# Kernel optimization log

Measured on AMD Instinct MI355X. Metric: run time of the kernel, lower is better.

Reference implementation:

```python
import jax, jax.numpy as jnp
import numpy as np

D = 1024
H = 16
HD = D // H

def setup_inputs() -> dict:
    key = jax.random.key(0)
    ks = jax.random.split(key, 5)
    scale = 1.0 / np.sqrt(D)
    x = jax.random.normal(ks[0], (2, 2048, D), dtype=jnp.float32)
    W_qkv = jax.random.uniform(ks[1], (D, 3 * D), minval=-scale, maxval=scale, dtype=jnp.float32)
    b_qkv = jax.random.uniform(ks[2], (3 * D,), minval=-scale, maxval=scale, dtype=jnp.float32)
    W_out = jax.random.uniform(ks[3], (D, D), minval=-scale, maxval=scale, dtype=jnp.float32)
    b_out = jax.random.uniform(ks[4], (D,), minval=-scale, maxval=scale, dtype=jnp.float32)
    return {"x": x, "W_qkv": W_qkv, "b_qkv": b_qkv, "W_out": W_out, "b_out": b_out}

def reference(x, W_qkv, b_qkv, W_out, b_out):
    B, S, _ = x.shape
    qkv = x @ W_qkv + b_qkv  # [B,S,3D]
    qkv = qkv.reshape(B, S, 3, H, HD).transpose(2, 0, 3, 1, 4)  # [3,B,H,S,HD]
    q, k, v = qkv[0], qkv[1], qkv[2]
    scores = jnp.einsum('bhsd,bhtd->bhst', q, k) / jnp.sqrt(jnp.float32(HD))
    probs = jax.nn.softmax(scores, axis=-1)
    attn = jnp.einsum('bhst,bhtd->bhsd', probs, v)  # [B,H,S,HD]
    attn = attn.transpose(0, 2, 1, 3).reshape(B, S, D)
    return attn @ W_out + b_out
```

## Files before the change

### kernel.cpp

```cpp
#include <hip/hip_runtime.h>


typedef short bf16x8 __attribute__((ext_vector_type(8)));
typedef short bf16x4 __attribute__((ext_vector_type(4)));
typedef float f32x4 __attribute__((ext_vector_type(4)));

#if __has_builtin(__builtin_amdgcn_mfma_f32_16x16x16_bf16)
#define MFMA16(a, b, c) __builtin_amdgcn_mfma_f32_16x16x16_bf16(a, b, c, 0, 0, 0)
#else
#define MFMA16(a, b, c) __builtin_amdgcn_mfma_f32_16x16x16bf16_1k(a, b, c, 0, 0, 0)
#endif

__device__ __forceinline__ unsigned short f2bf(float f) {
  unsigned u = __float_as_uint(f);
  u = (u + 0x7fffu + ((u >> 16) & 1u)) >> 16;
  return (unsigned short)u;
}
__device__ __forceinline__ unsigned pack_bf2(float lo, float hi) {
  unsigned a = __float_as_uint(lo) + 0x8000u;
  unsigned b = __float_as_uint(hi) + 0x8000u;
  return __builtin_amdgcn_perm(b, a, 0x07060302);
}
__device__ __forceinline__ void load_lds16(const unsigned short* g, unsigned short* l) {
  __builtin_amdgcn_global_load_lds(
      (const __attribute__((address_space(1))) void*)g,
      (__attribute__((address_space(3))) void*)l, 16, 0, 0);
}

__global__ __launch_bounds__(256) void cvt_f32_bf16(
    const float* __restrict__ in, unsigned short* __restrict__ out, int n)
{
  const int i = (blockIdx.x * 256 + threadIdx.x) * 8;
  if (i >= n) return;
  float4 f0 = *(const float4*)(in + i);
  float4 f1 = *(const float4*)(in + i + 4);
  union { unsigned short u[8]; uint4 v; } pk;
  pk.u[0] = f2bf(f0.x); pk.u[1] = f2bf(f0.y); pk.u[2] = f2bf(f0.z); pk.u[3] = f2bf(f0.w);
  pk.u[4] = f2bf(f1.x); pk.u[5] = f2bf(f1.y); pk.u[6] = f2bf(f1.z); pk.u[7] = f2bf(f1.w);
  *(uint4*)(out + i) = pk.v;
}

__global__ __launch_bounds__(256) void transpose_cvt(
    const float* __restrict__ in, unsigned short* __restrict__ out, int R, int C)
{
  __shared__ float tile[64][65];
  const int tid = threadIdx.x;
  const int r0 = blockIdx.y * 64, c0 = blockIdx.x * 64;
  {
    const int rr = tid >> 4;
    const int cc = (tid & 15) * 4;
#pragma unroll
    for (int it = 0; it < 4; ++it) {
      float4 f = *(const float4*)&in[(size_t)(r0 + rr + 16 * it) * C + c0 + cc];
      tile[rr + 16 * it][cc + 0] = f.x;
      tile[rr + 16 * it][cc + 1] = f.y;
      tile[rr + 16 * it][cc + 2] = f.z;
      tile[rr + 16 * it][cc + 3] = f.w;
    }
  }
  __syncthreads();
  {
    const int cr = tid >> 2;
    const int rk = (tid & 3) * 16;
    union { unsigned short u[16]; uint4 v[2]; } pk;
#pragma unroll
    for (int j = 0; j < 16; ++j) pk.u[j] = f2bf(tile[rk + j][cr]);
    uint4* dst = (uint4*)&out[(size_t)(c0 + cr) * R + r0 + rk];
    dst[0] = pk.v[0];
    dst[1] = pk.v[1];
  }
}

template <int MODE>
__global__ __launch_bounds__(256) void gemm_mfma(
    const unsigned short* __restrict__ A,
    const unsigned short* __restrict__ Bt,
    const float* __restrict__ bias,
    void* __restrict__ Cout, unsigned short* __restrict__ vT,
    int M, int N, int K)
{
  __shared__ unsigned short As[128][32];
  __shared__ unsigned short Bs[128][32];
  const int tid = threadIdx.x;
  const int wave = tid >> 6, lane = tid & 63;
  const int l16 = lane & 15, quad = lane >> 4;
  const int m0 = blockIdx.y * 128, n0 = blockIdx.x * 128;
  const int wm = (wave & 1) * 64, wn = (wave >> 1) * 64;
  const int lr = lane >> 2;
  const int lc = (lane & 3) * 8;

  f32x4 acc[4][4] = {};

  for (int k0 = 0; k0 < K; k0 += 32) {
    __syncthreads();
    load_lds16(&A [(size_t)(m0 + 16 * wave + lr) * K + k0 + lc],      &As[16 * wave][0]);
    load_lds16(&A [(size_t)(m0 + 64 + 16 * wave + lr) * K + k0 + lc], &As[64 + 16 * wave][0]);
    load_lds16(&Bt[(size_t)(n0 + 16 * wave + lr) * K + k0 + lc],      &Bs[16 * wave][0]);
    load_lds16(&Bt[(size_t)(n0 + 64 + 16 * wave + lr) * K + k0 + lc], &Bs[64 + 16 * wave][0]);
    __syncthreads();

    bf16x8 af[4], bfr[4];
#pragma unroll
    for (int mi = 0; mi < 4; ++mi)
      af[mi] = *(const bf16x8*)&As[wm + 16 * mi + l16][quad * 8];
#pragma unroll
    for (int ni = 0; ni < 4; ++ni)
      bfr[ni] = *(const bf16x8*)&Bs[wn + 16 * ni + l16][quad * 8];
#pragma unroll
    for (int mi = 0; mi < 4; ++mi)
#pragma unroll
      for (int ni = 0; ni < 4; ++ni)
        acc[mi][ni] = __builtin_amdgcn_mfma_f32_16x16x32_bf16(
            af[mi], bfr[ni], acc[mi][ni], 0, 0, 0);
  }

  const float SCQ = 0.18033688f;
#pragma unroll
  for (int ni = 0; ni < 4; ++ni) {
    const int colb = n0 + wn + 16 * ni;
    const int col = colb + l16;
    const float bv = bias[col];
    if (MODE == 0) {
#pragma unroll
      for (int mi = 0; mi < 4; ++mi)
#pragma unroll
        for (int i = 0; i < 4; ++i) {
          const int row = m0 + wm + 16 * mi + quad * 4 + i;
          ((float*)Cout)[(size_t)row * N + col] = acc[mi][ni][i] + bv;
        }
    } else if (colb < 1024) {
#pragma unroll
      for (int mi = 0; mi < 4; ++mi)
#pragma unroll
        for (int i = 0; i < 4; ++i) {
          const int row = m0 + wm + 16 * mi + quad * 4 + i;
          ((unsigned short*)Cout)[(size_t)row * N + col] = f2bf((acc[mi][ni][i] + bv) * SCQ);
        }
    } else if (colb < 2048) {
#pragma unroll
      for (int mi = 0; mi < 4; ++mi)
#pragma unroll
        for (int i = 0; i < 4; ++i) {
          const int row = m0 + wm + 16 * mi + quad * 4 + i;
          ((unsigned short*)Cout)[(size_t)row * N + col] = f2bf(acc[mi][ni][i] + bv);
        }
    } else {
      const int h = (col - 2048) >> 6, d = col & 63;
#pragma unroll
      for (int mi = 0; mi < 4; ++mi) {
        const int row = m0 + wm + 16 * mi + quad * 4;
        const int bb = row >> 11, t = row & 2047;
        unsigned short* dst = &vT[((size_t)(bb * 16 + h) * 64 + d) * 2048 + t];
        *(unsigned*)(dst)     = pack_bf2(acc[mi][ni][0] + bv, acc[mi][ni][1] + bv);
        *(unsigned*)(dst + 2) = pack_bf2(acc[mi][ni][2] + bv, acc[mi][ni][3] + bv);
      }
    }
  }
}

__global__ __launch_bounds__(256, 2) void attn_mfma(
    const unsigned short* __restrict__ qkv,
    const unsigned short* __restrict__ vT,
    unsigned short* __restrict__ attn_out)
{
  __shared__ unsigned short Ks[2][4096];
  __shared__ unsigned short Vs[2][4096];

  const int tid = threadIdx.x;
  const int wave = tid >> 6, lane = tid & 63;
  const int l16 = lane & 15, quad = lane >> 4;
  const int bh = blockIdx.y, b = bh >> 4, h = bh & 15;
  const int s0 = blockIdx.x * 128 + wave * 32;

  const unsigned short* qb = qkv + (size_t)(b * 2048) * 3072 + h * 64;
  const unsigned short* kb = qb + 1024;
  const unsigned short* vb = vT + (size_t)bh * 64 * 2048;

  const int srow = lane >> 3;
  const int schunk = ((lane & 7) ^ srow) * 8;
  const int r0a = wave * 16;
  const unsigned short* kg0 = kb + (size_t)(r0a + srow) * 3072 + schunk;
  const unsigned short* kg1 = kg0 + (size_t)8 * 3072;
  const unsigned short* vg0 = vb + (size_t)(r0a + srow) * 2048 + schunk;
  const unsigned short* vg1 = vg0 + (size_t)8 * 2048;

#define STAGE_KV(buf, t0)                                            \
  do {                                                               \
    load_lds16(kg0 + (size_t)(t0) * 3072, &Ks[buf][r0a * 64]);       \
    load_lds16(kg1 + (size_t)(t0) * 3072, &Ks[buf][(r0a + 8) * 64]); \
    load_lds16(vg0 + (t0),                &Vs[buf][r0a * 64]);       \
    load_lds16(vg1 + (t0),                &Vs[buf][(r0a + 8) * 64]); \
  } while (0)

  STAGE_KV(0, 0);

  bf16x8 qf[2][2];
#pragma unroll
  for (int mt = 0; mt < 2; ++mt)
#pragma unroll
    for (int ks = 0; ks < 2; ++ks)
      qf[mt][ks] = *(const bf16x8*)&qb[(size_t)(s0 + 16 * mt + l16) * 3072 + 32 * ks + quad * 8];

  f32x4 O[2][4] = {};
  f32x4 lacc[2] = {};
  const bf16x4 ones4 = {(short)0x3F80, (short)0x3F80, (short)0x3F80, (short)0x3F80};
  const int sw = l16 & 7;
  const int h2 = quad >> 1, h1 = (quad & 1) * 4;

  for (int it = 0; it < 32; ++it) {
    const int cur = it & 1;
    __syncthreads();
    if (it < 31) STAGE_KV(1 - cur, (it + 1) * 64);

    bf16x8 kf[4][2];
#pragma unroll
    for (int nt = 0; nt < 4; ++nt) {
      const int rb = (16 * nt + l16) * 64;
      kf[nt][0] = *(const bf16x8*)&Ks[cur][rb + ((quad ^ sw) * 8)];
      kf[nt][1] = *(const bf16x8*)&Ks[cur][rb + (((4 + quad) ^ sw) * 8)];
    }

    bf16x4 vf[4][4];
#pragma unroll
    for (int nd = 0; nd < 4; ++nd) {
      const int rb = (16 * nd + l16) * 64;
#pragma unroll
      for (int c = 0; c < 4; ++c)
        vf[nd][c] = *(const bf16x4*)&Vs[cur][rb + (((2 * c + h2) ^ sw) * 8 + h1)];
    }

    f32x4 sf[4][2];
#pragma unroll
    for (int nt = 0; nt < 4; ++nt)
#pragma unroll
      for (int mt = 0; mt < 2; ++mt) {
        f32x4 c = {0.0f, 0.0f, 0.0f, 0.0f};
        c = __builtin_amdgcn_mfma_f32_16x16x32_bf16(kf[nt][0], qf[mt][0], c, 0, 0, 0);
        c = __builtin_amdgcn_mfma_f32_16x16x32_bf16(kf[nt][1], qf[mt][1], c, 0, 0, 0);
        sf[nt][mt] = c;
      }

    bf16x4 pp[2][4];
#pragma unroll
    for (int mt = 0; mt < 2; ++mt)
#pragma unroll
      for (int nt = 0; nt < 4; ++nt) {
        const float p0 = __builtin_amdgcn_exp2f(sf[nt][mt][0]);
        const float p1 = __builtin_amdgcn_exp2f(sf[nt][mt][1]);
        const float p2 = __builtin_amdgcn_exp2f(sf[nt][mt][2]);
        const float p3 = __builtin_amdgcn_exp2f(sf[nt][mt][3]);
        uint2 w;
        w.x = pack_bf2(p0, p1);
        w.y = pack_bf2(p2, p3);
        pp[mt][nt] = *(bf16x4*)&w;
      }

#pragma unroll
    for (int c = 0; c < 4; ++c)
#pragma unroll
      for (int mt = 0; mt < 2; ++mt) {
        lacc[mt] = MFMA16(ones4, pp[mt][c], lacc[mt]);
#pragma unroll
        for (int nd = 0; nd < 4; ++nd)
          O[mt][nd] = MFMA16(vf[nd][c], pp[mt][c], O[mt][nd]);
      }
  }

#pragma unroll
  for (int mt = 0; mt < 2; ++mt) {
    const float inv = 1.0f / lacc[mt][0];
    const size_t row = (size_t)(b * 2048 + s0 + 16 * mt + l16);
#pragma unroll
    for (int nd = 0; nd < 4; ++nd) {
      uint2 w;
      w.x = pack_bf2(O[mt][nd][0] * inv, O[mt][nd][1] * inv);
      w.y = pack_bf2(O[mt][nd][2] * inv, O[mt][nd][3] * inv);
      *(uint2*)&attn_out[row * 1024 + h * 64 + 16 * nd + quad * 4] = w;
    }
  }
#undef STAGE_KV
}

extern "C" void kernel_launch(void* const* d_in, const int* in_sizes, int n_in,
                              void* d_out, int out_size, void* d_ws, size_t ws_size,
                              hipStream_t stream) {
  const float* x     = (const float*)d_in[0];
  const float* W_qkv = (const float*)d_in[1];
  const float* b_qkv = (const float*)d_in[2];
  const float* W_out = (const float*)d_in[3];
  const float* b_out = (const float*)d_in[4];
  float* out = (float*)d_out;

  char* ws = (char*)d_ws;
  unsigned short* x_bf   = (unsigned short*)(ws);
  unsigned short* Wqkv_t = (unsigned short*)(ws + 8388608);
  unsigned short* Wout_t = (unsigned short*)(ws + 14680064);
  unsigned short* qkv_bf = (unsigned short*)(ws + 16777216);
  unsigned short* vT     = (unsigned short*)(ws + 41943040);
  unsigned short* attn_b = (unsigned short*)(ws + 50331648);

  cvt_f32_bf16<<<2048, 256, 0, stream>>>(x, x_bf, 4096 * 1024);
  transpose_cvt<<<dim3(48, 16), 256, 0, stream>>>(W_qkv, Wqkv_t, 1024, 3072);
  transpose_cvt<<<dim3(16, 16), 256, 0, stream>>>(W_out, Wout_t, 1024, 1024);

  gemm_mfma<1><<<dim3(24, 32), 256, 0, stream>>>(x_bf, Wqkv_t, b_qkv, qkv_bf, vT,
                                                 4096, 3072, 1024);
  attn_mfma<<<dim3(16, 32), 256, 0, stream>>>(qkv_bf, vT, attn_b);
  gemm_mfma<0><<<dim3(8, 32), 256, 0, stream>>>(attn_b, Wout_t, b_out, out, nullptr,
                                                4096, 1024, 1024);
}
```

Baseline: 203.4 us.

## Split attention over key halves with merge kernel, compact QK buffer, fuse transposes

Attention is split along the key dimension into two halves (grid z=2), each writing unnormalized bf16 partial outputs and row sums. A new merge kernel adds them and normalizes. The aim is twice as many blocks for better CU occupancy. The occupancy hint rises to 4 blocks per SM. The QKV GEMM now writes only Q and K into a 2048-wide buffer, and the two weight transposes are fused into one launch. The costs are extra partial-buffer traffic, an extra kernel launch, and precision loss from storing partial sums in bf16. The merge is valid because the softmax here uses no max subtraction.

```diff
diff --git a/kernel.cpp b/kernel.cpp
--- a/kernel.cpp
+++ b/kernel.cpp
@@ -21,6 +21,8 @@
   unsigned b = __float_as_uint(hi) + 0x8000u;
   return __builtin_amdgcn_perm(b, a, 0x07060302);
 }
+__device__ __forceinline__ float bf_lo(unsigned u) { return __uint_as_float(u << 16); }
+__device__ __forceinline__ float bf_hi(unsigned u) { return __uint_as_float(u & 0xffff0000u); }
 __device__ __forceinline__ void load_lds16(const unsigned short* g, unsigned short* l) {
   __builtin_amdgcn_global_load_lds(
       (const __attribute__((address_space(1))) void*)g,
@@ -40,12 +42,19 @@
   *(uint4*)(out + i) = pk.v;
 }
 
-__global__ __launch_bounds__(256) void transpose_cvt(
-    const float* __restrict__ in, unsigned short* __restrict__ out, int R, int C)
-{
+__global__ __launch_bounds__(256) void transpose_cvt2(
+    const float* __restrict__ in0, unsigned short* __restrict__ out0, int R0, int C0,
+    const float* __restrict__ in1, unsigned short* __restrict__ out1, int R1, int C1)
+{
+  const float* in = (blockIdx.z == 0) ? in0 : in1;
+  unsigned short* out = (blockIdx.z == 0) ? out0 : out1;
+  const int R = (blockIdx.z == 0) ? R0 : R1;
+  const int C = (blockIdx.z == 0) ? C0 : C1;
+  const int c0 = blockIdx.x * 64;
+  if (c0 >= C) return;
   __shared__ float tile[64][65];
   const int tid = threadIdx.x;
-  const int r0 = blockIdx.y * 64, c0 = blockIdx.x * 64;
+  const int r0 = blockIdx.y * 64;
   {
     const int rr = tid >> 4;
     const int cc = (tid & 15) * 4;
@@ -77,7 +86,7 @@
     const unsigned short* __restrict__ Bt,
     const float* __restrict__ bias,
     void* __restrict__ Cout, unsigned short* __restrict__ vT,
-    int M, int N, int K)
+    int M, int N, int K, int ldc)
 {
   __shared__ unsigned short As[128][32];
   __shared__ unsigned short Bs[128][32];
@@ -126,7 +135,7 @@
 #pragma unroll
         for (int i = 0; i < 4; ++i) {
           const int row = m0 + wm + 16 * mi + quad * 4 + i;
-          ((float*)Cout)[(size_t)row * N + col] = acc[mi][ni][i] + bv;
+          ((float*)Cout)[(size_t)row * ldc + col] = acc[mi][ni][i] + bv;
         }
     } else if (colb < 1024) {
 #pragma unroll
@@ -134,7 +143,7 @@
 #pragma unroll
         for (int i = 0; i < 4; ++i) {
           const int row = m0 + wm + 16 * mi + quad * 4 + i;
-          ((unsigned short*)Cout)[(size_t)row * N + col] = f2bf((acc[mi][ni][i] + bv) * SCQ);
+          ((unsigned short*)Cout)[(size_t)row * ldc + col] = f2bf((acc[mi][ni][i] + bv) * SCQ);
         }
     } else if (colb < 2048) {
 #pragma unroll
@@ -142,7 +151,7 @@
 #pragma unroll
         for (int i = 0; i < 4; ++i) {
           const int row = m0 + wm + 16 * mi + quad * 4 + i;
-          ((unsigned short*)Cout)[(size_t)row * N + col] = f2bf(acc[mi][ni][i] + bv);
+          ((unsigned short*)Cout)[(size_t)row * ldc + col] = f2bf(acc[mi][ni][i] + bv);
         }
     } else {
       const int h = (col - 2048) >> 6, d = col & 63;
@@ -158,10 +167,11 @@
   }
 }
 
-__global__ __launch_bounds__(256, 2) void attn_mfma(
-    const unsigned short* __restrict__ qkv,
+__global__ __launch_bounds__(256, 4) void attn_mfma(
+    const unsigned short* __restrict__ qk,
     const unsigned short* __restrict__ vT,
-    unsigned short* __restrict__ attn_out)
+    unsigned short* __restrict__ Opart,
+    float* __restrict__ lpart)
 {
   __shared__ unsigned short Ks[2][4096];
   __shared__ unsigned short Vs[2][4096];
@@ -170,24 +180,26 @@
   const int wave = tid >> 6, lane = tid & 63;
   const int l16 = lane & 15, quad = lane >> 4;
   const int bh = blockIdx.y, b = bh >> 4, h = bh & 15;
+  const int tpar = blockIdx.z;
   const int s0 = blockIdx.x * 128 + wave * 32;
 
-  const unsigned short* qb = qkv + (size_t)(b * 2048) * 3072 + h * 64;
+  const unsigned short* qb = qk + (size_t)(b * 2048) * 2048 + h * 64;
   const unsigned short* kb = qb + 1024;
   const unsigned short* vb = vT + (size_t)bh * 64 * 2048;
 
   const int srow = lane >> 3;
   const int schunk = ((lane & 7) ^ srow) * 8;
   const int r0a = wave * 16;
-  const unsigned short* kg0 = kb + (size_t)(r0a + srow) * 3072 + schunk;
-  const unsigned short* kg1 = kg0 + (size_t)8 * 3072;
-  const unsigned short* vg0 = vb + (size_t)(r0a + srow) * 2048 + schunk;
+  const int tbase = tpar * 1024;
+  const unsigned short* kg0 = kb + (size_t)(tbase + r0a + srow) * 2048 + schunk;
+  const unsigned short* kg1 = kg0 + (size_t)8 * 2048;
+  const unsigned short* vg0 = vb + (size_t)(r0a + srow) * 2048 + tbase + schunk;
   const unsigned short* vg1 = vg0 + (size_t)8 * 2048;
 
 #define STAGE_KV(buf, t0)                                            \
   do {                                                               \
-    load_lds16(kg0 + (size_t)(t0) * 3072, &Ks[buf][r0a * 64]);       \
-    load_lds16(kg1 + (size_t)(t0) * 3072, &Ks[buf][(r0a + 8) * 64]); \
+    load_lds16(kg0 + (size_t)(t0) * 2048, &Ks[buf][r0a * 64]);       \
+    load_lds16(kg1 + (size_t)(t0) * 2048, &Ks[buf][(r0a + 8) * 64]); \
     load_lds16(vg0 + (t0),                &Vs[buf][r0a * 64]);       \
     load_lds16(vg1 + (t0),                &Vs[buf][(r0a + 8) * 64]); \
   } while (0)
@@ -199,7 +211,7 @@
   for (int mt = 0; mt < 2; ++mt)
 #pragma unroll
     for (int ks = 0; ks < 2; ++ks)
-      qf[mt][ks] = *(const bf16x8*)&qb[(size_t)(s0 + 16 * mt + l16) * 3072 + 32 * ks + quad * 8];
+      qf[mt][ks] = *(const bf16x8*)&qb[(size_t)(s0 + 16 * mt + l16) * 2048 + 32 * ks + quad * 8];
 
   f32x4 O[2][4] = {};
   f32x4 lacc[2] = {};
@@ -207,10 +219,10 @@
   const int sw = l16 & 7;
   const int h2 = quad >> 1, h1 = (quad & 1) * 4;
 
-  for (int it = 0; it < 32; ++it) {
+  for (int it = 0; it < 16; ++it) {
     const int cur = it & 1;
     __syncthreads();
-    if (it < 31) STAGE_KV(1 - cur, (it + 1) * 64);
+    if (it < 15) STAGE_KV(1 - cur, (it + 1) * 64);
 
     bf16x8 kf[4][2];
 #pragma unroll
@@ -268,17 +280,39 @@
 
 #pragma unroll
   for (int mt = 0; mt < 2; ++mt) {
-    const float inv = 1.0f / lacc[mt][0];
     const size_t row = (size_t)(b * 2048 + s0 + 16 * mt + l16);
+    unsigned short* dst = &Opart[((size_t)tpar * 4096 + row) * 1024 + h * 64];
 #pragma unroll
     for (int nd = 0; nd < 4; ++nd) {
       uint2 w;
-      w.x = pack_bf2(O[mt][nd][0] * inv, O[mt][nd][1] * inv);
-      w.y = pack_bf2(O[mt][nd][2] * inv, O[mt][nd][3] * inv);
-      *(uint2*)&attn_out[row * 1024 + h * 64 + 16 * nd + quad * 4] = w;
-    }
+      w.x = pack_bf2(O[mt][nd][0], O[mt][nd][1]);
+      w.y = pack_bf2(O[mt][nd][2], O[mt][nd][3]);
+      *(uint2*)&dst[16 * nd + quad * 4] = w;
+    }
+    if (quad == 0)
+      lpart[((size_t)tpar * 32 + bh) * 2048 + s0 + 16 * mt + l16] = lacc[mt][0];
   }
 #undef STAGE_KV
+}
+
+__global__ __launch_bounds__(256) void attn_merge(
+    const unsigned short* __restrict__ Opart,
+    const float* __restrict__ lpart,
+    unsigned short* __restrict__ attn_out)
+{
+  const int row = blockIdx.x;
+  const int c0 = threadIdx.x * 4;
+  const int b = row >> 11, s = row & 2047;
+  const int h = c0 >> 6;
+  const size_t li = (size_t)(b * 16 + h) * 2048 + s;
+  const float inv = 1.0f / (lpart[li] + lpart[65536 + li]);
+  const size_t oi = (size_t)row * 1024 + c0;
+  uint2 o0 = *(const uint2*)&Opart[oi];
+  uint2 o1 = *(const uint2*)&Opart[4194304 + oi];
+  uint2 w;
+  w.x = pack_bf2((bf_lo(o0.x) + bf_lo(o1.x)) * inv, (bf_hi(o0.x) + bf_hi(o1.x)) * inv);
+  w.y = pack_bf2((bf_lo(o0.y) + bf_lo(o1.y)) * inv, (bf_hi(o0.y) + bf_hi(o1.y)) * inv);
+  *(uint2*)&attn_out[oi] = w;
 }
 
 extern "C" void kernel_launch(void* const* d_in, const int* in_sizes, int n_in,
@@ -292,20 +326,24 @@
   float* out = (float*)d_out;
 
   char* ws = (char*)d_ws;
-  unsigned short* x_bf   = (unsigned short*)(ws);
-  unsigned short* Wqkv_t = (unsigned short*)(ws + 8388608);
-  unsigned short* Wout_t = (unsigned short*)(ws + 14680064);
-  unsigned short* qkv_bf = (unsigned short*)(ws + 16777216);
-  unsigned short* vT     = (unsigned short*)(ws + 41943040);
-  unsigned short* attn_b = (unsigned short*)(ws + 50331648);
+  const size_t MB = 1048576;
+  unsigned short* Wout_t = (unsigned short*)(ws);
+  unsigned short* qk_bf  = (unsigned short*)(ws + 2 * MB);
+  unsigned short* vT     = (unsigned short*)(ws + 18 * MB);
+  unsigned short* attn_b = (unsigned short*)(ws + 26 * MB);
+  unsigned short* x_bf   = (unsigned short*)(ws + 34 * MB);
+  float*          lpart  = (float*)(ws + 34 * MB);
+  unsigned short* Wqkv_t = (unsigned short*)(ws + 42 * MB);
+  unsigned short* Opart  = (unsigned short*)(ws + 48 * MB);
 
   cvt_f32_bf16<<<2048, 256, 0, stream>>>(x, x_bf, 4096 * 1024);
-  transpose_cvt<<<dim3(48, 16), 256, 0, stream>>>(W_qkv, Wqkv_t, 1024, 3072);
-  transpose_cvt<<<dim3(16, 16), 256, 0, stream>>>(W_out, Wout_t, 1024, 1024);
-
-  gemm_mfma<1><<<dim3(24, 32), 256, 0, stream>>>(x_bf, Wqkv_t, b_qkv, qkv_bf, vT,
-                                                 4096, 3072, 1024);
-  attn_mfma<<<dim3(16, 32), 256, 0, stream>>>(qkv_bf, vT, attn_b);
+  transpose_cvt2<<<dim3(48, 16, 2), 256, 0, stream>>>(
+      W_qkv, Wqkv_t, 1024, 3072, W_out, Wout_t, 1024, 1024);
+
+  gemm_mfma<1><<<dim3(24, 32), 256, 0, stream>>>(x_bf, Wqkv_t, b_qkv, qk_bf, vT,
+                                                 4096, 3072, 1024, 2048);
+  attn_mfma<<<dim3(16, 32, 2), 256, 0, stream>>>(qk_bf, vT, Opart, lpart);
+  attn_merge<<<4096, 256, 0, stream>>>(Opart, lpart, attn_b);
   gemm_mfma<0><<<dim3(8, 32), 256, 0, stream>>>(attn_b, Wout_t, b_out, out, nullptr,
-                                                4096, 1024, 1024);
-}
+                                                4096, 1024, 1024, 1024);
+}
```

New measurement: 208.9 us. 2.7% more time.

## Fuse prep kernels, compact QK buffer, register-staged KV prefetch in attention

Applied to the files above, without the earlier changes.

Merges the x conversion and both weight transposes into one launch, which removes two kernel launches. The QKV GEMM now writes only Q and K into a buffer with a 2048 stride, since V already goes to the transposed buffer, and the workspace is re-laid out to match. Attention drops async global-to-LDS loads in favour of register-staged prefetch two tiles ahead: each iteration writes the next tile to LDS after the QK MFMAs, with one barrier per iteration. This adds register pressure and may overlap loads with compute less well than the async path did.

```diff
diff --git a/kernel.cpp b/kernel.cpp
--- a/kernel.cpp
+++ b/kernel.cpp
@@ -27,25 +27,33 @@
       (__attribute__((address_space(3))) void*)l, 16, 0, 0);
 }
 
-__global__ __launch_bounds__(256) void cvt_f32_bf16(
-    const float* __restrict__ in, unsigned short* __restrict__ out, int n)
+__global__ __launch_bounds__(256) void prep(
+    const float* __restrict__ x, unsigned short* __restrict__ x_bf,
+    const float* __restrict__ W_qkv, unsigned short* __restrict__ Wqkv_t,
+    const float* __restrict__ W_out, unsigned short* __restrict__ Wout_t)
 {
-  const int i = (blockIdx.x * 256 + threadIdx.x) * 8;
-  if (i >= n) return;
-  float4 f0 = *(const float4*)(in + i);
-  float4 f1 = *(const float4*)(in + i + 4);
-  union { unsigned short u[8]; uint4 v; } pk;
-  pk.u[0] = f2bf(f0.x); pk.u[1] = f2bf(f0.y); pk.u[2] = f2bf(f0.z); pk.u[3] = f2bf(f0.w);
-  pk.u[4] = f2bf(f1.x); pk.u[5] = f2bf(f1.y); pk.u[6] = f2bf(f1.z); pk.u[7] = f2bf(f1.w);
-  *(uint4*)(out + i) = pk.v;
-}
-
-__global__ __launch_bounds__(256) void transpose_cvt(
-    const float* __restrict__ in, unsigned short* __restrict__ out, int R, int C)
-{
+  const int tid = threadIdx.x;
+  if (blockIdx.z == 2) {
+    const int bid = blockIdx.y * 48 + blockIdx.x;
+    const int n = 4096 * 1024;
+    for (int i = bid * 2048 + tid * 8; i < n; i += 768 * 2048) {
+      float4 f0 = *(const float4*)(x + i);
+      float4 f1 = *(const float4*)(x + i + 4);
+      union { unsigned short u[8]; uint4 v; } pk;
+      pk.u[0] = f2bf(f0.x); pk.u[1] = f2bf(f0.y); pk.u[2] = f2bf(f0.z); pk.u[3] = f2bf(f0.w);
+      pk.u[4] = f2bf(f1.x); pk.u[5] = f2bf(f1.y); pk.u[6] = f2bf(f1.z); pk.u[7] = f2bf(f1.w);
+      *(uint4*)(x_bf + i) = pk.v;
+    }
+    return;
+  }
+  const float* in = (blockIdx.z == 0) ? W_qkv : W_out;
+  unsigned short* out = (blockIdx.z == 0) ? Wqkv_t : Wout_t;
+  const int R = 1024;
+  const int C = (blockIdx.z == 0) ? 3072 : 1024;
+  const int c0 = blockIdx.x * 64;
+  if (c0 >= C) return;
   __shared__ float tile[64][65];
-  const int tid = threadIdx.x;
-  const int r0 = blockIdx.y * 64, c0 = blockIdx.x * 64;
+  const int r0 = blockIdx.y * 64;
   {
     const int rr = tid >> 4;
     const int cc = (tid & 15) * 4;
@@ -77,7 +85,7 @@
     const unsigned short* __restrict__ Bt,
     const float* __restrict__ bias,
     void* __restrict__ Cout, unsigned short* __restrict__ vT,
-    int M, int N, int K)
+    int M, int N, int K, int ldc)
 {
   __shared__ unsigned short As[128][32];
   __shared__ unsigned short Bs[128][32];
@@ -126,7 +134,7 @@
 #pragma unroll
         for (int i = 0; i < 4; ++i) {
           const int row = m0 + wm + 16 * mi + quad * 4 + i;
-          ((float*)Cout)[(size_t)row * N + col] = acc[mi][ni][i] + bv;
+          ((float*)Cout)[(size_t)row * ldc + col] = acc[mi][ni][i] + bv;
         }
     } else if (colb < 1024) {
 #pragma unroll
@@ -134,7 +142,7 @@
 #pragma unroll
         for (int i = 0; i < 4; ++i) {
           const int row = m0 + wm + 16 * mi + quad * 4 + i;
-          ((unsigned short*)Cout)[(size_t)row * N + col] = f2bf((acc[mi][ni][i] + bv) * SCQ);
+          ((unsigned short*)Cout)[(size_t)row * ldc + col] = f2bf((acc[mi][ni][i] + bv) * SCQ);
         }
     } else if (colb < 2048) {
 #pragma unroll
@@ -142,7 +150,7 @@
 #pragma unroll
         for (int i = 0; i < 4; ++i) {
           const int row = m0 + wm + 16 * mi + quad * 4 + i;
-          ((unsigned short*)Cout)[(size_t)row * N + col] = f2bf(acc[mi][ni][i] + bv);
+          ((unsigned short*)Cout)[(size_t)row * ldc + col] = f2bf(acc[mi][ni][i] + bv);
         }
     } else {
       const int h = (col - 2048) >> 6, d = col & 63;
@@ -159,7 +167,7 @@
 }
 
 __global__ __launch_bounds__(256, 2) void attn_mfma(
-    const unsigned short* __restrict__ qkv,
+    const unsigned short* __restrict__ qk,
     const unsigned short* __restrict__ vT,
     unsigned short* __restrict__ attn_out)
 {
@@ -172,34 +180,37 @@
   const int bh = blockIdx.y, b = bh >> 4, h = bh & 15;
   const int s0 = blockIdx.x * 128 + wave * 32;
 
-  const unsigned short* qb = qkv + (size_t)(b * 2048) * 3072 + h * 64;
+  const unsigned short* qb = qk + (size_t)(b * 2048) * 2048 + h * 64;
   const unsigned short* kb = qb + 1024;
   const unsigned short* vb = vT + (size_t)bh * 64 * 2048;
 
   const int srow = lane >> 3;
   const int schunk = ((lane & 7) ^ srow) * 8;
   const int r0a = wave * 16;
-  const unsigned short* kg0 = kb + (size_t)(r0a + srow) * 3072 + schunk;
-  const unsigned short* kg1 = kg0 + (size_t)8 * 3072;
+  const unsigned short* kg0 = kb + (size_t)(r0a + srow) * 2048 + schunk;
+  const unsigned short* kg1 = kg0 + (size_t)8 * 2048;
   const unsigned short* vg0 = vb + (size_t)(r0a + srow) * 2048 + schunk;
   const unsigned short* vg1 = vg0 + (size_t)8 * 2048;
-
-#define STAGE_KV(buf, t0)                                            \
-  do {                                                               \
-    load_lds16(kg0 + (size_t)(t0) * 3072, &Ks[buf][r0a * 64]);       \
-    load_lds16(kg1 + (size_t)(t0) * 3072, &Ks[buf][(r0a + 8) * 64]); \
-    load_lds16(vg0 + (t0),                &Vs[buf][r0a * 64]);       \
-    load_lds16(vg1 + (t0),                &Vs[buf][(r0a + 8) * 64]); \
-  } while (0)
-
-  STAGE_KV(0, 0);
+  const int wd0 = r0a * 64 + lane * 8;
+  const int wd1 = (r0a + 8) * 64 + lane * 8;
+
+  uint4 kr0 = *(const uint4*)(kg0);
+  uint4 kr1 = *(const uint4*)(kg1);
+  uint4 vr0 = *(const uint4*)(vg0);
+  uint4 vr1 = *(const uint4*)(vg1);
+  *(uint4*)&Ks[0][wd0] = kr0;  *(uint4*)&Ks[0][wd1] = kr1;
+  *(uint4*)&Vs[0][wd0] = vr0;  *(uint4*)&Vs[0][wd1] = vr1;
+  kr0 = *(const uint4*)(kg0 + (size_t)64 * 2048);
+  kr1 = *(const uint4*)(kg1 + (size_t)64 * 2048);
+  vr0 = *(const uint4*)(vg0 + 64);
+  vr1 = *(const uint4*)(vg1 + 64);
 
   bf16x8 qf[2][2];
 #pragma unroll
   for (int mt = 0; mt < 2; ++mt)
 #pragma unroll
     for (int ks = 0; ks < 2; ++ks)
-      qf[mt][ks] = *(const bf16x8*)&qb[(size_t)(s0 + 16 * mt + l16) * 3072 + 32 * ks + quad * 8];
+      qf[mt][ks] = *(const bf16x8*)&qb[(size_t)(s0 + 16 * mt + l16) * 2048 + 32 * ks + quad * 8];
 
   f32x4 O[2][4] = {};
   f32x4 lacc[2] = {};
@@ -207,10 +218,10 @@
   const int sw = l16 & 7;
   const int h2 = quad >> 1, h1 = (quad & 1) * 4;
 
+  __syncthreads();
+
   for (int it = 0; it < 32; ++it) {
     const int cur = it & 1;
-    __syncthreads();
-    if (it < 31) STAGE_KV(1 - cur, (it + 1) * 64);
 
     bf16x8 kf[4][2];
 #pragma unroll
@@ -218,15 +229,6 @@
       const int rb = (16 * nt + l16) * 64;
       kf[nt][0] = *(const bf16x8*)&Ks[cur][rb + ((quad ^ sw) * 8)];
       kf[nt][1] = *(const bf16x8*)&Ks[cur][rb + (((4 + quad) ^ sw) * 8)];
-    }
-
-    bf16x4 vf[4][4];
-#pragma unroll
-    for (int nd = 0; nd < 4; ++nd) {
-      const int rb = (16 * nd + l16) * 64;
-#pragma unroll
-      for (int c = 0; c < 4; ++c)
-        vf[nd][c] = *(const bf16x4*)&Vs[cur][rb + (((2 * c + h2) ^ sw) * 8 + h1)];
     }
 
     f32x4 sf[4][2];
@@ -239,6 +241,29 @@
         c = __builtin_amdgcn_mfma_f32_16x16x32_bf16(kf[nt][1], qf[mt][1], c, 0, 0, 0);
         sf[nt][mt] = c;
       }
+
+    if (it < 31) {
+      *(uint4*)&Ks[cur ^ 1][wd0] = kr0;
+      *(uint4*)&Ks[cur ^ 1][wd1] = kr1;
+      *(uint4*)&Vs[cur ^ 1][wd0] = vr0;
+      *(uint4*)&Vs[cur ^ 1][wd1] = vr1;
+      if (it < 30) {
+        const size_t ko = (size_t)(it + 2) * 64 * 2048;
+        kr0 = *(const uint4*)(kg0 + ko);
+        kr1 = *(const uint4*)(kg1 + ko);
+        vr0 = *(const uint4*)(vg0 + (it + 2) * 64);
+        vr1 = *(const uint4*)(vg1 + (it + 2) * 64);
+      }
+    }
+
+    bf16x4 vf[4][4];
+#pragma unroll
+    for (int nd = 0; nd < 4; ++nd) {
+      const int rb = (16 * nd + l16) * 64;
+#pragma unroll
+      for (int c = 0; c < 4; ++c)
+        vf[nd][c] = *(const bf16x4*)&Vs[cur][rb + (((2 * c + h2) ^ sw) * 8 + h1)];
+    }
 
     bf16x4 pp[2][4];
 #pragma unroll
@@ -264,6 +289,8 @@
         for (int nd = 0; nd < 4; ++nd)
           O[mt][nd] = MFMA16(vf[nd][c], pp[mt][c], O[mt][nd]);
       }
+
+    __syncthreads();
   }
 
 #pragma unroll
@@ -278,7 +305,6 @@
       *(uint2*)&attn_out[row * 1024 + h * 64 + 16 * nd + quad * 4] = w;
     }
   }
-#undef STAGE_KV
 }
 
 extern "C" void kernel_launch(void* const* d_in, const int* in_sizes, int n_in,
@@ -292,20 +318,19 @@
   float* out = (float*)d_out;
 
   char* ws = (char*)d_ws;
-  unsigned short* x_bf   = (unsigned short*)(ws);
-  unsigned short* Wqkv_t = (unsigned short*)(ws + 8388608);
-  unsigned short* Wout_t = (unsigned short*)(ws + 14680064);
-  unsigned short* qkv_bf = (unsigned short*)(ws + 16777216);
-  unsigned short* vT     = (unsigned short*)(ws + 41943040);
-  unsigned short* attn_b = (unsigned short*)(ws + 50331648);
-
-  cvt_f32_bf16<<<2048, 256, 0, stream>>>(x, x_bf, 4096 * 1024);
-  transpose_cvt<<<dim3(48, 16), 256, 0, stream>>>(W_qkv, Wqkv_t, 1024, 3072);
-  transpose_cvt<<<dim3(16, 16), 256, 0, stream>>>(W_out, Wout_t, 1024, 1024);
-
-  gemm_mfma<1><<<dim3(24, 32), 256, 0, stream>>>(x_bf, Wqkv_t, b_qkv, qkv_bf, vT,
-                                                 4096, 3072, 1024);
-  attn_mfma<<<dim3(16, 32), 256, 0, stream>>>(qkv_bf, vT, attn_b);
+  const size_t MB = 1048576;
+  unsigned short* Wout_t = (unsigned short*)(ws);
+  unsigned short* qk_bf  = (unsigned short*)(ws + 2 * MB);
+  unsigned short* vT     = (unsigned short*)(ws + 18 * MB);
+  unsigned short* attn_b = (unsigned short*)(ws + 26 * MB);
+  unsigned short* x_bf   = (unsigned short*)(ws + 34 * MB);
+  unsigned short* Wqkv_t = (unsigned short*)(ws + 42 * MB);
+
+  prep<<<dim3(48, 16, 3), 256, 0, stream>>>(x, x_bf, W_qkv, Wqkv_t, W_out, Wout_t);
+
+  gemm_mfma<1><<<dim3(24, 32), 256, 0, stream>>>(x_bf, Wqkv_t, b_qkv, qk_bf, vT,
+                                                 4096, 3072, 1024, 2048);
+  attn_mfma<<<dim3(16, 32), 256, 0, stream>>>(qk_bf, vT, attn_b);
   gemm_mfma<0><<<dim3(8, 32), 256, 0, stream>>>(attn_b, Wout_t, b_out, out, nullptr,
-                                                4096, 1024, 1024);
-}
+                                                4096, 1024, 1024, 1024);
+}
```

New measurement: 196.0 us. -3.6%, faster.
